# Optimization experiments

Measured on AMD Instinct MI355X. Metric: run time of the kernel, lower is better.

Reference implementation:

```python
import jax, jax.numpy as jnp
import numpy as np

N_NODES = 50000
N_EDGES = 800000
DIM = 128
NEG_SLOPE = 0.01  # nn.LeakyReLU default


def setup_inputs() -> dict:
    key = jax.random.key(0)
    ks = jax.random.split(key, 9)
    src = jax.random.randint(ks[0], (N_EDGES,), 0, N_NODES, dtype=jnp.int32)
    dst = jax.random.randint(ks[1], (N_EDGES,), 0, N_NODES, dtype=jnp.int32)
    weight = jax.random.normal(ks[2], (N_NODES,), dtype=jnp.float32)
    significance = jax.random.randint(ks[3], (N_NODES,), 0, 2, dtype=jnp.int32)
    emb = jax.random.normal(ks[4], (2, 2), dtype=jnp.float32) * 0.1
    W0 = jax.random.normal(ks[5], (3, DIM), dtype=jnp.float32) * (1.0 / np.sqrt(3))
    b0 = jnp.zeros((DIM,), dtype=jnp.float32)
    W1 = jax.random.normal(ks[6], (DIM, DIM), dtype=jnp.float32) * (1.0 / np.sqrt(DIM))
    b1 = jnp.zeros((DIM,), dtype=jnp.float32)
    return {"src": src, "dst": dst, "weight": weight, "significance": significance,
            "emb": emb, "W0": W0, "b0": b0, "W1": W1, "b1": b1}


def _graph_conv(src, dst, x, W, b, n_nodes):
    # DGL GraphConv, norm='both', allow_zero_in_degree=True:
    # h = D_in^{-1/2} A D_out^{-1/2} x W + b, degrees clamped to >= 1.
    ones = jnp.ones(src.shape[0], dtype=x.dtype)
    out_deg = jnp.clip(jax.ops.segment_sum(ones, src, num_segments=n_nodes), 1.0)
    in_deg = jnp.clip(jax.ops.segment_sum(ones, dst, num_segments=n_nodes), 1.0)
    h = x * (out_deg ** -0.5)[:, None]            # [N, d] scale src side
    agg = jax.ops.segment_sum(h[src], dst, num_segments=n_nodes)  # gather+scatter over edges
    agg = agg * (in_deg ** -0.5)[:, None]
    return agg @ W + b


def reference(src, dst, weight, significance, emb, W0, b0, W1, b1):
    n_nodes = weight.shape[0]
    sig = emb[significance]                        # [N, 2] embedding lookup
    feats = jnp.concatenate([weight[:, None], sig], axis=1)  # [N, 3]
    h = _graph_conv(src, dst, feats, W0, b0, n_nodes)        # conv_0
    h = jax.nn.leaky_relu(h, negative_slope=NEG_SLOPE)
    h = _graph_conv(src, dst, h, W1, b1, n_nodes)            # layers[0]
    return h
```

## Files before the change

kernel.cpp:

```cpp
#include <hip/hip_runtime.h>

#define N_NODES 50000
#define N_EDGES 800000
#define DIM 128
#define NEG_SLOPE 0.01f
#define CAP 32
#define OVF_MAX 4096

#define NR 4
#define RNODES 12512
#define SLICES 64
#define ESLICE (N_EDGES / SLICES)

__device__ inline unsigned f2b_rne2(float a, float b) {
    unsigned ua = __float_as_uint(a), ub = __float_as_uint(b);
    ua = (ua + 0x7fffu + ((ua >> 16) & 1u)) >> 16;
    ub = (ub + 0x7fffu + ((ub >> 16) & 1u)) >> 16;
    return ua | (ub << 16);
}
__device__ inline float b2f_lo(unsigned u) { return __uint_as_float(u << 16); }
__device__ inline float b2f_hi(unsigned u) { return __uint_as_float(u & 0xffff0000u); }

__global__ __launch_bounds__(512) void k_hist2(const int* __restrict__ src,
                                               const int* __restrict__ dst,
                                               int* __restrict__ pSrc, int* __restrict__ pDst) {
    __shared__ int bs[RNODES];
    __shared__ int bd[RNODES];
    int range = blockIdx.x / SLICES;
    int slice = blockIdx.x % SLICES;
    int tid = threadIdx.x;
    for (int j = tid; j < RNODES; j += 512) { bs[j] = 0; bd[j] = 0; }
    __syncthreads();
    int base = range * RNODES;
    const int4* s4 = (const int4*)(src + slice * ESLICE);
    const int4* d4 = (const int4*)(dst + slice * ESLICE);
    for (int t = tid; t < ESLICE / 4; t += 512) {
        int4 v = s4[t];
        unsigned u0 = (unsigned)(v.x - base), u1 = (unsigned)(v.y - base);
        unsigned u2 = (unsigned)(v.z - base), u3 = (unsigned)(v.w - base);
        if (u0 < RNODES) atomicAdd(&bs[u0], 1);
        if (u1 < RNODES) atomicAdd(&bs[u1], 1);
        if (u2 < RNODES) atomicAdd(&bs[u2], 1);
        if (u3 < RNODES) atomicAdd(&bs[u3], 1);
        int4 w = d4[t];
        unsigned w0 = (unsigned)(w.x - base), w1 = (unsigned)(w.y - base);
        unsigned w2 = (unsigned)(w.z - base), w3 = (unsigned)(w.w - base);
        if (w0 < RNODES) atomicAdd(&bd[w0], 1);
        if (w1 < RNODES) atomicAdd(&bd[w1], 1);
        if (w2 < RNODES) atomicAdd(&bd[w2], 1);
        if (w3 < RNODES) atomicAdd(&bd[w3], 1);
    }
    __syncthreads();
    int* os = pSrc + (size_t)blockIdx.x * RNODES;
    int* od = pDst + (size_t)blockIdx.x * RNODES;
    for (int j = tid; j < RNODES; j += 512) { os[j] = bs[j]; od[j] = bd[j]; }
}

__global__ void k_scanprep(const float* __restrict__ weight, const int* __restrict__ sig,
                           const float* __restrict__ emb,
                           const int* __restrict__ pSrc, int* __restrict__ pDst,
                           int* __restrict__ icnt, float* __restrict__ oinv,
                           float* __restrict__ iinv, float* __restrict__ feats3,
                           int* __restrict__ ovf_cnt, int n) {
    int g = blockIdx.x * blockDim.x + threadIdx.x;
    if (g == 0) *ovf_cnt = 0;
    if (g >= NR * RNODES) return;
    int range = g / RNODES, off = g % RNODES;
    size_t basei = (size_t)(range * SLICES) * RNODES + off;
    int run = 0;
    #pragma unroll 8
    for (int s = 0; s < SLICES; ++s) {
        size_t idx = basei + (size_t)s * RNODES;
        int c = pDst[idx];
        pDst[idx] = run;
        run += c;
    }
    int od = 0;
    #pragma unroll 8
    for (int s = 0; s < SLICES; ++s) od += pSrc[basei + (size_t)s * RNODES];
    if (g < n) {
        icnt[g] = run;
        float oi = 1.0f / sqrtf((float)max(od, 1));
        oinv[g] = oi;
        iinv[g] = 1.0f / sqrtf((float)max(run, 1));
        int sg = sig[g];
        feats3[g * 3 + 0] = weight[g] * oi;
        feats3[g * 3 + 1] = emb[sg * 2 + 0] * oi;
        feats3[g * 3 + 2] = emb[sg * 2 + 1] * oi;
    }
}

__global__ __launch_bounds__(512) void k_fill3(const int* __restrict__ src,
                                               const int* __restrict__ dst,
                                               const int* __restrict__ pDst,
                                               unsigned short* __restrict__ eidx,
                                               int* __restrict__ ovf_cnt, int2* __restrict__ ovf) {
    __shared__ int cur[RNODES];
    int range = blockIdx.x / SLICES;
    int slice = blockIdx.x % SLICES;
    int tid = threadIdx.x;
    const int* pr = pDst + (size_t)blockIdx.x * RNODES;
    for (int j = tid; j < RNODES; j += 512) cur[j] = pr[j];
    __syncthreads();
    int base = range * RNODES;
    const int* ss = src + slice * ESLICE;
    const int* dd = dst + slice * ESLICE;
    for (int t = tid; t < ESLICE; t += 512) {
        int d = dd[t];
        unsigned u = (unsigned)(d - base);
        if (u < RNODES) {
            int s = ss[t];
            int p = atomicAdd(&cur[u], 1);
            if (p < CAP) eidx[(size_t)d * CAP + p] = (unsigned short)s;
            else { int o = atomicAdd(ovf_cnt, 1); if (o < OVF_MAX) ovf[o] = make_int2(d, s); }
        }
    }
}

__global__ void k_aggl1(const int* __restrict__ icnt, const unsigned short* __restrict__ eidx,
                        const float* __restrict__ feats3,
                        const int* __restrict__ ovf_cnt, const int2* __restrict__ ovf,
                        const float* __restrict__ iinv, const float* __restrict__ oinv,
                        const float* __restrict__ W0, const float* __restrict__ b0,
                        uint4* __restrict__ hs, int n) {
    int t = blockIdx.x * blockDim.x + threadIdx.x;
    int i = t >> 4;
    if (i >= n) return;
    int q = t & 15;
    int ic = icnt[i];
    int deg = min(ic, CAP);
    const unsigned short* row = eidx + (size_t)i * CAP;
    float a0 = 0.f, a1 = 0.f, a2 = 0.f;
    for (int k = q; k < deg; k += 16) {
        int s = row[k];
        a0 += feats3[s * 3 + 0];
        a1 += feats3[s * 3 + 1];
        a2 += feats3[s * 3 + 2];
    }
    if (ic > CAP) {
        int cnt = min(*ovf_cnt, OVF_MAX);
        for (int e = q; e < cnt; e += 16) {
            int2 ov = ovf[e];
            if (ov.x == i) {
                a0 += feats3[ov.y * 3 + 0];
                a1 += feats3[ov.y * 3 + 1];
                a2 += feats3[ov.y * 3 + 2];
            }
        }
    }
    #pragma unroll
    for (int m = 1; m <= 8; m <<= 1) {
        a0 += __shfl_xor(a0, m);
        a1 += __shfl_xor(a1, m);
        a2 += __shfl_xor(a2, m);
    }
    float ii = iinv[i], oi = oinv[i];
    a0 *= ii; a1 *= ii; a2 *= ii;
    int j0 = q * 8;
    float v[8];
    #pragma unroll
    for (int c = 0; c < 8; ++c) {
        float x = a0 * W0[j0 + c] + a1 * W0[DIM + j0 + c] + a2 * W0[2 * DIM + j0 + c]
                + b0[j0 + c];
        v[c] = x > 0.f ? x : NEG_SLOPE * x;
    }
    hs[i * 16 + q] = make_uint4(f2b_rne2(v[0] * oi, v[1] * oi),
                                f2b_rne2(v[2] * oi, v[3] * oi),
                                f2b_rne2(v[4] * oi, v[5] * oi),
                                f2b_rne2(v[6] * oi, v[7] * oi));
}

__global__ void k_gather128(const int* __restrict__ icnt, const unsigned short* __restrict__ eidx,
                            const uint4* __restrict__ hs,
                            const int* __restrict__ ovf_cnt, const int2* __restrict__ ovf,
                            float* __restrict__ agg, int n) {
    int t = blockIdx.x * blockDim.x + threadIdx.x;
    int i = t >> 4;
    if (i >= n) return;
    int q = t & 15;
    int ic = icnt[i];
    int deg = min(ic, CAP);
    const unsigned short* row = eidx + (size_t)i * CAP;
    float a0 = 0.f, a1 = 0.f, a2 = 0.f, a3 = 0.f;
    float a4 = 0.f, a5 = 0.f, a6 = 0.f, a7 = 0.f;
    int k = 0;
    for (; k + 8 <= deg; k += 8) {
        int s0 = row[k + 0], s1 = row[k + 1], s2 = row[k + 2], s3 = row[k + 3];
        int s4 = row[k + 4], s5 = row[k + 5], s6 = row[k + 6], s7 = row[k + 7];
        uint4 u0 = hs[s0 * 16 + q];
        uint4 u1 = hs[s1 * 16 + q];
        uint4 u2 = hs[s2 * 16 + q];
        uint4 u3 = hs[s3 * 16 + q];
        uint4 u4 = hs[s4 * 16 + q];
        uint4 u5 = hs[s5 * 16 + q];
        uint4 u6 = hs[s6 * 16 + q];
        uint4 u7 = hs[s7 * 16 + q];
        a0 += (b2f_lo(u0.x) + b2f_lo(u1.x)) + (b2f_lo(u2.x) + b2f_lo(u3.x))
            + (b2f_lo(u4.x) + b2f_lo(u5.x)) + (b2f_lo(u6.x) + b2f_lo(u7.x));
        a1 += (b2f_hi(u0.x) + b2f_hi(u1.x)) + (b2f_hi(u2.x) + b2f_hi(u3.x))
            + (b2f_hi(u4.x) + b2f_hi(u5.x)) + (b2f_hi(u6.x) + b2f_hi(u7.x));
        a2 += (b2f_lo(u0.y) + b2f_lo(u1.y)) + (b2f_lo(u2.y) + b2f_lo(u3.y))
            + (b2f_lo(u4.y) + b2f_lo(u5.y)) + (b2f_lo(u6.y) + b2f_lo(u7.y));
        a3 += (b2f_hi(u0.y) + b2f_hi(u1.y)) + (b2f_hi(u2.y) + b2f_hi(u3.y))
            + (b2f_hi(u4.y) + b2f_hi(u5.y)) + (b2f_hi(u6.y) + b2f_hi(u7.y));
        a4 += (b2f_lo(u0.z) + b2f_lo(u1.z)) + (b2f_lo(u2.z) + b2f_lo(u3.z))
            + (b2f_lo(u4.z) + b2f_lo(u5.z)) + (b2f_lo(u6.z) + b2f_lo(u7.z));
        a5 += (b2f_hi(u0.z) + b2f_hi(u1.z)) + (b2f_hi(u2.z) + b2f_hi(u3.z))
            + (b2f_hi(u4.z) + b2f_hi(u5.z)) + (b2f_hi(u6.z) + b2f_hi(u7.z));
        a6 += (b2f_lo(u0.w) + b2f_lo(u1.w)) + (b2f_lo(u2.w) + b2f_lo(u3.w))
            + (b2f_lo(u4.w) + b2f_lo(u5.w)) + (b2f_lo(u6.w) + b2f_lo(u7.w));
        a7 += (b2f_hi(u0.w) + b2f_hi(u1.w)) + (b2f_hi(u2.w) + b2f_hi(u3.w))
            + (b2f_hi(u4.w) + b2f_hi(u5.w)) + (b2f_hi(u6.w) + b2f_hi(u7.w));
    }
    for (; k < deg; ++k) {
        int s = row[k];
        uint4 u = hs[s * 16 + q];
        a0 += b2f_lo(u.x); a1 += b2f_hi(u.x);
        a2 += b2f_lo(u.y); a3 += b2f_hi(u.y);
        a4 += b2f_lo(u.z); a5 += b2f_hi(u.z);
        a6 += b2f_lo(u.w); a7 += b2f_hi(u.w);
    }
    if (ic > CAP) {
        int cnt = min(*ovf_cnt, OVF_MAX);
        for (int e = 0; e < cnt; ++e) {
            int2 ov = ovf[e];
            if (ov.x == i) {
                uint4 u = hs[ov.y * 16 + q];
                a0 += b2f_lo(u.x); a1 += b2f_hi(u.x);
                a2 += b2f_lo(u.y); a3 += b2f_hi(u.y);
                a4 += b2f_lo(u.z); a5 += b2f_hi(u.z);
                a6 += b2f_lo(u.w); a7 += b2f_hi(u.w);
            }
        }
    }
    ((float4*)agg)[(size_t)i * 32 + q * 2 + 0] = make_float4(a0, a1, a2, a3);
    ((float4*)agg)[(size_t)i * 32 + q * 2 + 1] = make_float4(a4, a5, a6, a7);
}

#define FB_NODES 128
__global__ __launch_bounds__(256) void k_final(const float* __restrict__ iinv,
                                               const float* __restrict__ W1,
                                               const float* __restrict__ b1,
                                               const float* __restrict__ agg,
                                               float* __restrict__ out, int n) {
    __shared__ float sW[DIM * 64];
    int tid = threadIdx.x;
    int half = blockIdx.x & 1;
    int tile = blockIdx.x >> 1;
    for (int idx = tid; idx < DIM * 64 / 4; idx += 256) {
        int r = idx >> 4, c4 = idx & 15;
        *(float4*)&sW[r * 64 + c4 * 4] = *(const float4*)&W1[r * DIM + half * 64 + c4 * 4];
    }
    int cg = tid & 15;
    int ng = tid >> 4;
    int col0 = cg * 4;
    int row0 = tile * FB_NODES + ng * 8;

    float acc[8][4];
    #pragma unroll
    for (int i = 0; i < 8; ++i)
        #pragma unroll
        for (int j = 0; j < 4; ++j) acc[i][j] = 0.f;

    __syncthreads();

    const float4* agg4 = (const float4*)agg;
    #pragma unroll 2
    for (int k4 = 0; k4 < 32; ++k4) {
        float4 a[8];
        #pragma unroll
        for (int i = 0; i < 8; ++i) {
            int r = min(row0 + i, n - 1);
            a[i] = agg4[(size_t)r * 32 + k4];
        }
        #pragma unroll
        for (int kk = 0; kk < 4; ++kk) {
            float4 w = *(const float4*)&sW[(k4 * 4 + kk) * 64 + col0];
            #pragma unroll
            for (int i = 0; i < 8; ++i) {
                float av = (kk == 0) ? a[i].x : (kk == 1) ? a[i].y : (kk == 2) ? a[i].z : a[i].w;
                acc[i][0] += av * w.x;
                acc[i][1] += av * w.y;
                acc[i][2] += av * w.z;
                acc[i][3] += av * w.w;
            }
        }
    }

    int gcol = half * 64 + col0;
    float4 bb = *(const float4*)&b1[gcol];
    #pragma unroll
    for (int i = 0; i < 8; ++i) {
        int r = row0 + i;
        if (r < n) {
            float ii = iinv[r];
            float4 o;
            o.x = acc[i][0] * ii + bb.x;
            o.y = acc[i][1] * ii + bb.y;
            o.z = acc[i][2] * ii + bb.z;
            o.w = acc[i][3] * ii + bb.w;
            ((float4*)out)[(size_t)r * 32 + (gcol >> 2)] = o;
        }
    }
}

extern "C" void kernel_launch(void* const* d_in, const int* in_sizes, int n_in,
                              void* d_out, int out_size, void* d_ws, size_t ws_size,
                              hipStream_t stream) {
    const int*   src  = (const int*)d_in[0];
    const int*   dst  = (const int*)d_in[1];
    const float* weight = (const float*)d_in[2];
    const int*   sig  = (const int*)d_in[3];
    const float* emb  = (const float*)d_in[4];
    const float* W0   = (const float*)d_in[5];
    const float* b0   = (const float*)d_in[6];
    const float* W1   = (const float*)d_in[7];
    const float* b1   = (const float*)d_in[8];
    float* out = (float*)d_out;

    int*   ovf_cnt = (int*)d_ws;
    int2*  ovf     = (int2*)(ovf_cnt + 8);
    int*   icnt    = (int*)(ovf + OVF_MAX);
    float* oinv    = (float*)(icnt + N_NODES);
    float* iinv    = oinv + N_NODES;
    float* feats3  = iinv + N_NODES;
    int*   pSrc    = (int*)(feats3 + 3 * N_NODES);
    int*   pDst    = pSrc + (size_t)NR * SLICES * RNODES;
    unsigned short* eidx = (unsigned short*)(pDst + (size_t)NR * SLICES * RNODES);
    uint4* hs      = (uint4*)(eidx + (size_t)N_NODES * CAP);
    float* aggbuf  = (float*)(hs + (size_t)N_NODES * 16);

    k_hist2<<<NR * SLICES, 512, 0, stream>>>(src, dst, pSrc, pDst);
    k_scanprep<<<(NR * RNODES + 255) / 256, 256, 0, stream>>>(weight, sig, emb, pSrc, pDst,
                                                              icnt, oinv, iinv, feats3,
                                                              ovf_cnt, N_NODES);
    k_fill3<<<NR * SLICES, 512, 0, stream>>>(src, dst, pDst, eidx, ovf_cnt, ovf);
    k_aggl1<<<(N_NODES * 16 + 255) / 256, 256, 0, stream>>>(icnt, eidx, feats3,
                                                            ovf_cnt, ovf, iinv, oinv,
                                                            W0, b0, hs, N_NODES);
    k_gather128<<<((N_NODES * 16) + 255) / 256, 256, 0, stream>>>(icnt, eidx, hs,
                                                                  ovf_cnt, ovf, aggbuf,
                                                                  N_NODES);
    k_final<<<((N_NODES + FB_NODES - 1) / FB_NODES) * 2, 256, 0, stream>>>(
        iinv, W1, b1, aggbuf, out, N_NODES);
}
```

Baseline: 137.4 us.

## Fuse second-layer gather with W1 matmul in one kernel via shared staging

Merges the layer-2 gather kernel and the final dense transform into a single kernel. Each block gathers 16 nodes' aggregated features into shared memory, scales them by the in-degree norm, then multiplies by W1 read straight from global memory (16 threads per node, 8 output columns each). This drops the 25.6 MB fp32 agg buffer round trip and one launch. The cost is that the W1 GEMM now reads W1 from global/L2 per block, with low per-thread reuse, instead of using a register-tiled, shared-memory W1.

```diff
diff --git a/kernel.cpp b/kernel.cpp
--- a/kernel.cpp
+++ b/kernel.cpp
@@ -170,137 +170,101 @@
                                 f2b_rne2(v[6] * oi, v[7] * oi));
 }
 
-__global__ void k_gather128(const int* __restrict__ icnt, const unsigned short* __restrict__ eidx,
-                            const uint4* __restrict__ hs,
-                            const int* __restrict__ ovf_cnt, const int2* __restrict__ ovf,
-                            float* __restrict__ agg, int n) {
-    int t = blockIdx.x * blockDim.x + threadIdx.x;
-    int i = t >> 4;
-    if (i >= n) return;
-    int q = t & 15;
-    int ic = icnt[i];
-    int deg = min(ic, CAP);
-    const unsigned short* row = eidx + (size_t)i * CAP;
+#define NPB 16
+#define SA_LD 132
+__global__ __launch_bounds__(256) void k_gfinal(
+        const int* __restrict__ icnt, const unsigned short* __restrict__ eidx,
+        const uint4* __restrict__ hs,
+        const int* __restrict__ ovf_cnt, const int2* __restrict__ ovf,
+        const float* __restrict__ iinv, const float* __restrict__ W1,
+        const float* __restrict__ b1, float* __restrict__ out, int n) {
+    __shared__ float sA[NPB][SA_LD];
+    int tid = threadIdx.x;
+    int q = tid & 15, nn = tid >> 4;
+    int i = blockIdx.x * NPB + nn;
+
     float a0 = 0.f, a1 = 0.f, a2 = 0.f, a3 = 0.f;
     float a4 = 0.f, a5 = 0.f, a6 = 0.f, a7 = 0.f;
-    int k = 0;
-    for (; k + 8 <= deg; k += 8) {
-        int s0 = row[k + 0], s1 = row[k + 1], s2 = row[k + 2], s3 = row[k + 3];
-        int s4 = row[k + 4], s5 = row[k + 5], s6 = row[k + 6], s7 = row[k + 7];
-        uint4 u0 = hs[s0 * 16 + q];
-        uint4 u1 = hs[s1 * 16 + q];
-        uint4 u2 = hs[s2 * 16 + q];
-        uint4 u3 = hs[s3 * 16 + q];
-        uint4 u4 = hs[s4 * 16 + q];
-        uint4 u5 = hs[s5 * 16 + q];
-        uint4 u6 = hs[s6 * 16 + q];
-        uint4 u7 = hs[s7 * 16 + q];
-        a0 += (b2f_lo(u0.x) + b2f_lo(u1.x)) + (b2f_lo(u2.x) + b2f_lo(u3.x))
-            + (b2f_lo(u4.x) + b2f_lo(u5.x)) + (b2f_lo(u6.x) + b2f_lo(u7.x));
-        a1 += (b2f_hi(u0.x) + b2f_hi(u1.x)) + (b2f_hi(u2.x) + b2f_hi(u3.x))
-            + (b2f_hi(u4.x) + b2f_hi(u5.x)) + (b2f_hi(u6.x) + b2f_hi(u7.x));
-        a2 += (b2f_lo(u0.y) + b2f_lo(u1.y)) + (b2f_lo(u2.y) + b2f_lo(u3.y))
-            + (b2f_lo(u4.y) + b2f_lo(u5.y)) + (b2f_lo(u6.y) + b2f_lo(u7.y));
-        a3 += (b2f_hi(u0.y) + b2f_hi(u1.y)) + (b2f_hi(u2.y) + b2f_hi(u3.y))
-            + (b2f_hi(u4.y) + b2f_hi(u5.y)) + (b2f_hi(u6.y) + b2f_hi(u7.y));
-        a4 += (b2f_lo(u0.z) + b2f_lo(u1.z)) + (b2f_lo(u2.z) + b2f_lo(u3.z))
-            + (b2f_lo(u4.z) + b2f_lo(u5.z)) + (b2f_lo(u6.z) + b2f_lo(u7.z));
-        a5 += (b2f_hi(u0.z) + b2f_hi(u1.z)) + (b2f_hi(u2.z) + b2f_hi(u3.z))
-            + (b2f_hi(u4.z) + b2f_hi(u5.z)) + (b2f_hi(u6.z) + b2f_hi(u7.z));
-        a6 += (b2f_lo(u0.w) + b2f_lo(u1.w)) + (b2f_lo(u2.w) + b2f_lo(u3.w))
-            + (b2f_lo(u4.w) + b2f_lo(u5.w)) + (b2f_lo(u6.w) + b2f_lo(u7.w));
-        a7 += (b2f_hi(u0.w) + b2f_hi(u1.w)) + (b2f_hi(u2.w) + b2f_hi(u3.w))
-            + (b2f_hi(u4.w) + b2f_hi(u5.w)) + (b2f_hi(u6.w) + b2f_hi(u7.w));
-    }
-    for (; k < deg; ++k) {
-        int s = row[k];
-        uint4 u = hs[s * 16 + q];
-        a0 += b2f_lo(u.x); a1 += b2f_hi(u.x);
-        a2 += b2f_lo(u.y); a3 += b2f_hi(u.y);
-        a4 += b2f_lo(u.z); a5 += b2f_hi(u.z);
-        a6 += b2f_lo(u.w); a7 += b2f_hi(u.w);
-    }
-    if (ic > CAP) {
-        int cnt = min(*ovf_cnt, OVF_MAX);
-        for (int e = 0; e < cnt; ++e) {
-            int2 ov = ovf[e];
-            if (ov.x == i) {
-                uint4 u = hs[ov.y * 16 + q];
-                a0 += b2f_lo(u.x); a1 += b2f_hi(u.x);
-                a2 += b2f_lo(u.y); a3 += b2f_hi(u.y);
-                a4 += b2f_lo(u.z); a5 += b2f_hi(u.z);
-                a6 += b2f_lo(u.w); a7 += b2f_hi(u.w);
+    if (i < n) {
+        int ic = icnt[i];
+        int deg = min(ic, CAP);
+        const unsigned short* row = eidx + (size_t)i * CAP;
+        int k = 0;
+        for (; k + 8 <= deg; k += 8) {
+            int s0 = row[k + 0], s1 = row[k + 1], s2 = row[k + 2], s3 = row[k + 3];
+            int s4 = row[k + 4], s5 = row[k + 5], s6 = row[k + 6], s7 = row[k + 7];
+            uint4 u0 = hs[s0 * 16 + q];
+            uint4 u1 = hs[s1 * 16 + q];
+            uint4 u2 = hs[s2 * 16 + q];
+            uint4 u3 = hs[s3 * 16 + q];
+            uint4 u4 = hs[s4 * 16 + q];
+            uint4 u5 = hs[s5 * 16 + q];
+            uint4 u6 = hs[s6 * 16 + q];
+            uint4 u7 = hs[s7 * 16 + q];
+            a0 += (b2f_lo(u0.x) + b2f_lo(u1.x)) + (b2f_lo(u2.x) + b2f_lo(u3.x))
+                + (b2f_lo(u4.x) + b2f_lo(u5.x)) + (b2f_lo(u6.x) + b2f_lo(u7.x));
+            a1 += (b2f_hi(u0.x) + b2f_hi(u1.x)) + (b2f_hi(u2.x) + b2f_hi(u3.x))
+                + (b2f_hi(u4.x) + b2f_hi(u5.x)) + (b2f_hi(u6.x) + b2f_hi(u7.x));
+            a2 += (b2f_lo(u0.y) + b2f_lo(u1.y)) + (b2f_lo(u2.y) + b2f_lo(u3.y))
+                + (b2f_lo(u4.y) + b2f_lo(u5.y)) + (b2f_lo(u6.y) + b2f_lo(u7.y));
+            a3 += (b2f_hi(u0.y) + b2f_hi(u1.y)) + (b2f_hi(u2.y) + b2f_hi(u3.y))
+                + (b2f_hi(u4.y) + b2f_hi(u5.y)) + (b2f_hi(u6.y) + b2f_hi(u7.y));
+            a4 += (b2f_lo(u0.z) + b2f_lo(u1.z)) + (b2f_lo(u2.z) + b2f_lo(u3.z))
+                + (b2f_lo(u4.z) + b2f_lo(u5.z)) + (b2f_lo(u6.z) + b2f_lo(u7.z));
+            a5 += (b2f_hi(u0.z) + b2f_hi(u1.z)) + (b2f_hi(u2.z) + b2f_hi(u3.z))
+                + (b2f_hi(u4.z) + b2f_hi(u5.z)) + (b2f_hi(u6.z) + b2f_hi(u7.z));
+            a6 += (b2f_lo(u0.w) + b2f_lo(u1.w)) + (b2f_lo(u2.w) + b2f_lo(u3.w))
+                + (b2f_lo(u4.w) + b2f_lo(u5.w)) + (b2f_lo(u6.w) + b2f_lo(u7.w));
+            a7 += (b2f_hi(u0.w) + b2f_hi(u1.w)) + (b2f_hi(u2.w) + b2f_hi(u3.w))
+                + (b2f_hi(u4.w) + b2f_hi(u5.w)) + (b2f_hi(u6.w) + b2f_hi(u7.w));
+        }
+        for (; k < deg; ++k) {
+            int s = row[k];
+            uint4 u = hs[s * 16 + q];
+            a0 += b2f_lo(u.x); a1 += b2f_hi(u.x);
+            a2 += b2f_lo(u.y); a3 += b2f_hi(u.y);
+            a4 += b2f_lo(u.z); a5 += b2f_hi(u.z);
+            a6 += b2f_lo(u.w); a7 += b2f_hi(u.w);
+        }
+        if (ic > CAP) {
+            int cnt = min(*ovf_cnt, OVF_MAX);
+            for (int e = 0; e < cnt; ++e) {
+                int2 ov = ovf[e];
+                if (ov.x == i) {
+                    uint4 u = hs[ov.y * 16 + q];
+                    a0 += b2f_lo(u.x); a1 += b2f_hi(u.x);
+                    a2 += b2f_lo(u.y); a3 += b2f_hi(u.y);
+                    a4 += b2f_lo(u.z); a5 += b2f_hi(u.z);
+                    a6 += b2f_lo(u.w); a7 += b2f_hi(u.w);
+                }
             }
         }
-    }
-    ((float4*)agg)[(size_t)i * 32 + q * 2 + 0] = make_float4(a0, a1, a2, a3);
-    ((float4*)agg)[(size_t)i * 32 + q * 2 + 1] = make_float4(a4, a5, a6, a7);
-}
-
-#define FB_NODES 128
-__global__ __launch_bounds__(256) void k_final(const float* __restrict__ iinv,
-                                               const float* __restrict__ W1,
-                                               const float* __restrict__ b1,
-                                               const float* __restrict__ agg,
-                                               float* __restrict__ out, int n) {
-    __shared__ float sW[DIM * 64];
-    int tid = threadIdx.x;
-    int half = blockIdx.x & 1;
-    int tile = blockIdx.x >> 1;
-    for (int idx = tid; idx < DIM * 64 / 4; idx += 256) {
-        int r = idx >> 4, c4 = idx & 15;
-        *(float4*)&sW[r * 64 + c4 * 4] = *(const float4*)&W1[r * DIM + half * 64 + c4 * 4];
-    }
-    int cg = tid & 15;
-    int ng = tid >> 4;
-    int col0 = cg * 4;
-    int row0 = tile * FB_NODES + ng * 8;
-
-    float acc[8][4];
-    #pragma unroll
-    for (int i = 0; i < 8; ++i)
-        #pragma unroll
-        for (int j = 0; j < 4; ++j) acc[i][j] = 0.f;
-
+        float ii = iinv[i];
+        a0 *= ii; a1 *= ii; a2 *= ii; a3 *= ii;
+        a4 *= ii; a5 *= ii; a6 *= ii; a7 *= ii;
+    }
+    *(float4*)&sA[nn][q * 8 + 0] = make_float4(a0, a1, a2, a3);
+    *(float4*)&sA[nn][q * 8 + 4] = make_float4(a4, a5, a6, a7);
     __syncthreads();
 
-    const float4* agg4 = (const float4*)agg;
-    #pragma unroll 2
-    for (int k4 = 0; k4 < 32; ++k4) {
-        float4 a[8];
-        #pragma unroll
-        for (int i = 0; i < 8; ++i) {
-            int r = min(row0 + i, n - 1);
-            a[i] = agg4[(size_t)r * 32 + k4];
-        }
-        #pragma unroll
-        for (int kk = 0; kk < 4; ++kk) {
-            float4 w = *(const float4*)&sW[(k4 * 4 + kk) * 64 + col0];
-            #pragma unroll
-            for (int i = 0; i < 8; ++i) {
-                float av = (kk == 0) ? a[i].x : (kk == 1) ? a[i].y : (kk == 2) ? a[i].z : a[i].w;
-                acc[i][0] += av * w.x;
-                acc[i][1] += av * w.y;
-                acc[i][2] += av * w.z;
-                acc[i][3] += av * w.w;
-            }
-        }
-    }
-
-    int gcol = half * 64 + col0;
-    float4 bb = *(const float4*)&b1[gcol];
-    #pragma unroll
-    for (int i = 0; i < 8; ++i) {
-        int r = row0 + i;
-        if (r < n) {
-            float ii = iinv[r];
-            float4 o;
-            o.x = acc[i][0] * ii + bb.x;
-            o.y = acc[i][1] * ii + bb.y;
-            o.z = acc[i][2] * ii + bb.z;
-            o.w = acc[i][3] * ii + bb.w;
-            ((float4*)out)[(size_t)r * 32 + (gcol >> 2)] = o;
-        }
+    float c0 = 0.f, c1 = 0.f, c2 = 0.f, c3 = 0.f;
+    float c4 = 0.f, c5 = 0.f, c6 = 0.f, c7 = 0.f;
+    const float4* W14 = (const float4*)W1;
+    #pragma unroll 4
+    for (int k = 0; k < DIM; ++k) {
+        float av = sA[nn][k];
+        float4 w0 = W14[k * 32 + q * 2 + 0];
+        float4 w1 = W14[k * 32 + q * 2 + 1];
+        c0 += av * w0.x; c1 += av * w0.y; c2 += av * w0.z; c3 += av * w0.w;
+        c4 += av * w1.x; c5 += av * w1.y; c6 += av * w1.z; c7 += av * w1.w;
+    }
+    if (i < n) {
+        float4 bb0 = *(const float4*)&b1[q * 8 + 0];
+        float4 bb1 = *(const float4*)&b1[q * 8 + 4];
+        ((float4*)out)[(size_t)i * 32 + q * 2 + 0] =
+            make_float4(c0 + bb0.x, c1 + bb0.y, c2 + bb0.z, c3 + bb0.w);
+        ((float4*)out)[(size_t)i * 32 + q * 2 + 1] =
+            make_float4(c4 + bb1.x, c5 + bb1.y, c6 + bb1.z, c7 + bb1.w);
     }
 }
 
@@ -328,7 +292,6 @@
     int*   pDst    = pSrc + (size_t)NR * SLICES * RNODES;
     unsigned short* eidx = (unsigned short*)(pDst + (size_t)NR * SLICES * RNODES);
     uint4* hs      = (uint4*)(eidx + (size_t)N_NODES * CAP);
-    float* aggbuf  = (float*)(hs + (size_t)N_NODES * 16);
 
     k_hist2<<<NR * SLICES, 512, 0, stream>>>(src, dst, pSrc, pDst);
     k_scanprep<<<(NR * RNODES + 255) / 256, 256, 0, stream>>>(weight, sig, emb, pSrc, pDst,
@@ -338,9 +301,7 @@
     k_aggl1<<<(N_NODES * 16 + 255) / 256, 256, 0, stream>>>(icnt, eidx, feats3,
                                                             ovf_cnt, ovf, iinv, oinv,
                                                             W0, b0, hs, N_NODES);
-    k_gather128<<<((N_NODES * 16) + 255) / 256, 256, 0, stream>>>(icnt, eidx, hs,
-                                                                  ovf_cnt, ovf, aggbuf,
-                                                                  N_NODES);
-    k_final<<<((N_NODES + FB_NODES - 1) / FB_NODES) * 2, 256, 0, stream>>>(
-        iinv, W1, b1, aggbuf, out, N_NODES);
-}
+    k_gfinal<<<(N_NODES + NPB - 1) / NPB, 256, 0, stream>>>(icnt, eidx, hs,
+                                                            ovf_cnt, ovf, iinv,
+                                                            W1, b1, out, N_NODES);
+}
```

Result: slower. 175.9 us (+28.0%).
